# Kernel tuning notes

Measured on AMD Instinct MI355X. Metric: run time of the kernel, lower is better.

The kernel has to match this reference:

```python
import jax, jax.numpy as jnp
import numpy as np

OUT_SIZE = 7
SPATIAL_SCALE = 0.0625
SAMPLE_NUM = 2


def setup_inputs() -> dict:
    key = jax.random.key(0)
    k1, k2, k3, k4, k5, k6 = jax.random.split(key, 6)
    N, C, H, W = 4, 256, 96, 96
    K = 1024
    features = jax.random.normal(k1, (N, C, H, W), dtype=jnp.float32)
    img_h, img_w = H / SPATIAL_SCALE, W / SPATIAL_SCALE
    batch_idx = jax.random.randint(k2, (K,), 0, N).astype(jnp.float32)
    x1 = jax.random.uniform(k3, (K,)) * (img_w - 320.0)
    y1 = jax.random.uniform(k4, (K,)) * (img_h - 320.0)
    x2 = x1 + 16.0 + jax.random.uniform(k5, (K,)) * 300.0
    y2 = y1 + 16.0 + jax.random.uniform(k6, (K,)) * 300.0
    rois = jnp.stack([batch_idx, x1, y1, x2, y2], axis=1).astype(jnp.float32)
    return {"features": features, "rois": rois}


def _sample_coords(start, bin_size):
    # start, bin_size: [K]; returns [K, OUT_SIZE*SAMPLE_NUM] sample-point coords
    g = jnp.arange(OUT_SIZE * SAMPLE_NUM, dtype=jnp.float32)
    bin_idx = jnp.floor(g / SAMPLE_NUM)
    sub = g - bin_idx * SAMPLE_NUM
    offs = bin_idx + (sub + 0.5) / SAMPLE_NUM
    return start[:, None] + bin_size[:, None] * offs[None, :]


def _interp_1d(coord, size):
    # coord: [K, G] sample coords along one axis of a map of length `size`.
    valid = (coord >= -1.0) & (coord <= jnp.float32(size))
    c = jnp.clip(coord, 0.0, jnp.float32(size - 1))
    lo = jnp.floor(c)
    hi = jnp.minimum(lo + 1.0, jnp.float32(size - 1))
    frac = c - lo  # weight of hi; (1-frac) weight of lo
    return lo.astype(jnp.int32), hi.astype(jnp.int32), frac, valid


def roi_align(features, rois):
    N, C, H, W = features.shape
    b = rois[:, 0].astype(jnp.int32)
    x1, y1, x2, y2 = (rois[:, i] * SPATIAL_SCALE for i in (1, 2, 3, 4))
    roi_w = jnp.maximum(x2 - x1, 1.0)
    roi_h = jnp.maximum(y2 - y1, 1.0)
    bin_w = roi_w / OUT_SIZE
    bin_h = roi_h / OUT_SIZE

    ys = _sample_coords(y1, bin_h)  # [K, G]
    xs = _sample_coords(x1, bin_w)  # [K, G]
    ylo, yhi, fy, vy = _interp_1d(ys, H)
    xlo, xhi, fx, vx = _interp_1d(xs, W)

    bb = b[:, None, None]

    def gather(yi, xi):
        # -> [K, G, G, C]
        return features[bb, :, yi[:, :, None], xi[:, None, :]]

    wy_lo, wy_hi = (1.0 - fy), fy
    wx_lo, wx_hi = (1.0 - fx), fx

    def w2(wy, wx):
        return (wy[:, :, None] * wx[:, None, :])[..., None]

    val = (gather(ylo, xlo) * w2(wy_lo, wx_lo)
           + gather(ylo, xhi) * w2(wy_lo, wx_hi)
           + gather(yhi, xlo) * w2(wy_hi, wx_lo)
           + gather(yhi, xhi) * w2(wy_hi, wx_hi))
    mask = (vy[:, :, None] & vx[:, None, :])[..., None]
    val = jnp.where(mask, val, 0.0)

    K = rois.shape[0]
    G = OUT_SIZE * SAMPLE_NUM
    val = val.reshape(K, OUT_SIZE, SAMPLE_NUM, OUT_SIZE, SAMPLE_NUM, C)
    out = val.mean(axis=(2, 4))          # average the sample points per bin
    return jnp.transpose(out, (0, 3, 1, 2))  # [K, C, out, out]


def reference(features, rois):
    return roi_align(features, rois)
```

## Files before the change

kernel.cpp:

```cpp
#include <hip/hip_runtime.h>

#define CCH   256
#define FH    96
#define FW    96
#define HW    (FH*FW)
#define SCALE 0.0625f

#define HROWS 21
#define PSTR  28
#define PLANE (HROWS*PSTR)
#define WCH   32

__global__ __launch_bounds__(256, 8)
void roialign_kernel(const float* __restrict__ feat,
                     const float* __restrict__ rois,
                     float* __restrict__ out)
{
    __shared__ __align__(16) float win[4 * PLANE];
    __shared__ int   s_lo[2][14];
    __shared__ float s_wl[2][14], s_wh[2][14];

    const int k    = blockIdx.x >> 1;
    const int half = blockIdx.x & 1;
    const int tid  = threadIdx.x;
    const int w    = tid >> 6;
    const int ll   = tid & 63;

    const float x1 = rois[k*5+1] * SCALE;
    const float y1 = rois[k*5+2] * SCALE;
    const float x2 = rois[k*5+3] * SCALE;
    const float y2 = rois[k*5+4] * SCALE;
    const int   b  = (int)rois[k*5+0];
    const float binw = fmaxf(x2 - x1, 1.0f) * (1.0f/7.0f);
    const float binh = fmaxf(y2 - y1, 1.0f) * (1.0f/7.0f);

    if (tid < 28) {
        const int   axis  = (tid >= 14) ? 1 : 0;
        const int   g     = axis ? tid - 14 : tid;
        const float start = axis ? x1 : y1;
        const float bsz   = axis ? binw : binh;
        const float offs  = (float)(g >> 1) + 0.25f + 0.5f*(float)(g & 1);
        const float coord = start + bsz * offs;
        const bool  valid = (coord >= -1.0f) && (coord <= 96.0f);
        const float cc    = fminf(fmaxf(coord, 0.0f), 95.0f);
        const float lof   = floorf(cc);
        const float frac  = cc - lof;
        const float v     = valid ? 1.0f : 0.0f;
        s_lo[axis][g] = (int)lof;
        s_wl[axis][g] = (1.0f - frac) * v;
        s_wh[axis][g] = frac * v;
    }
    __syncthreads();

    const int row0 = s_lo[0][0];
    const int col0 = min(s_lo[1][0] & ~3, FW - 24);
    int hw_        = min(s_lo[0][13] + 1, FH-1) - row0 + 1;
    const int hwin = min(hw_, HROWS);
    const int nslot = hwin * 6;

    float* const wp = &win[w * PLANE];

    {
        const float4 z = make_float4(0.f, 0.f, 0.f, 0.f);
        #pragma unroll
        for (int j = 0; j < 3; ++j) {
            const int q = ll + 64*j;
            if (q < PLANE/4) *(float4*)&wp[q*4] = z;
        }
    }

    const bool active = ll < 49;
    const int  p  = active ? ll : 0;
    const int  oy = p / 7;
    const int  ox = p - oy*7;

    int   aL[4], aH[4];
    float w00[4], w01[4], w10[4], w11[4];
    #pragma unroll
    for (int sy = 0; sy < 2; ++sy) {
        const int   gy  = 2*oy + sy;
        const int   rlo = min(s_lo[0][gy] - row0,                 HROWS-1);
        const int   rhi = min(min(s_lo[0][gy]+1, FH-1) - row0,    HROWS-1);
        const float wyl = s_wl[0][gy], wyh = s_wh[0][gy];
        #pragma unroll
        for (int sx = 0; sx < 2; ++sx) {
            const int   gx  = 2*ox + sx;
            const int   clo = min(s_lo[1][gx] - col0, PSTR-2);
            const float wxl = s_wl[1][gx], wxh = s_wh[1][gx];
            const int   s   = sy*2 + sx;
            aL[s] = rlo*PSTR + clo;
            aH[s] = rhi*PSTR + clo;
            w00[s] = wyl*wxl*0.25f;  w01[s] = wyl*wxh*0.25f;
            w10[s] = wyh*wxl*0.25f;  w11[s] = wyh*wxh*0.25f;
        }
    }

    const int  sl1 = ll + 64;
    const int  r0  = ll  / 6, q0 = ll  - r0*6;
    const int  r1  = sl1 / 6, q1 = sl1 - r1*6;
    const bool L0  = ll  < nslot;
    const bool L1  = sl1 < nslot;
    const int  goff0 = min(row0 + r0, FH-1)*FW + col0 + q0*4;
    const int  goff1 = min(row0 + r1, FH-1)*FW + col0 + q1*4;
    const int  ld0   = min(r0, HROWS-1)*PSTR + q0*4;
    const int  ld1   = min(r1, HROWS-1)*PSTR + q1*4;

    const int    cb   = half*128 + w*WCH;
    const float* gch  = feat + (size_t)(b*CCH + cb) * HW;
    float*       outp = out  + ((size_t)k*CCH + cb)*49 + p;

    float4 st0, st1;
    if (L0) st0 = *(const float4*)(gch + goff0);
    if (L1) st1 = *(const float4*)(gch + goff1);

    for (int c = 0; c < WCH; ++c) {
        if (L0) *(float4*)&wp[ld0] = st0;
        if (L1) *(float4*)&wp[ld1] = st1;

        if (c + 1 < WCH) {
            const float* gn = gch + (size_t)(c+1)*HW;
            if (L0) st0 = *(const float4*)(gn + goff0);
            if (L1) st1 = *(const float4*)(gn + goff1);
        }

        if (active) {
            float acc = 0.0f;
            #pragma unroll
            for (int s = 0; s < 4; ++s) {
                acc += w00[s]*wp[aL[s]]   + w01[s]*wp[aL[s]+1]
                     + w10[s]*wp[aH[s]]   + w11[s]*wp[aH[s]+1];
            }
            outp[0] = acc;
        }
        outp += 49;
    }
}

extern "C" void kernel_launch(void* const* d_in, const int* in_sizes, int n_in,
                              void* d_out, int out_size, void* d_ws, size_t ws_size,
                              hipStream_t stream) {
    const float* feat = (const float*)d_in[0];
    const float* rois = (const float*)d_in[1];
    float*       outp = (float*)d_out;
    const int K = in_sizes[1] / 5;
    roialign_kernel<<<K*2, 256, 0, stream>>>(feat, rois, outp);
}
```

Baseline: 134.9 us.

## Prefetch four channels ahead, remap workgroups across XCDs, relax launch bounds

Each wave now keeps four channel windows in flight in registers instead of one, so global loads for later channels overlap the shared-memory store and bilinear compute of the current one. The per-channel sum is split into four independent partial sums to shorten the dependency chain. Workgroup IDs are remapped so that consecutive IDs, which round-robin across XCDs, are assigned to ROI/half pairs grouped per XCD. Launch bounds drop from 8 to 6 waves to leave room for the extra registers. The remap formula hardcodes K=1024, and the register pressure may lower occupancy.

```diff
diff --git a/kernel.cpp b/kernel.cpp
--- a/kernel.cpp
+++ b/kernel.cpp
@@ -11,7 +11,7 @@
 #define PLANE (HROWS*PSTR)
 #define WCH   32
 
-__global__ __launch_bounds__(256, 8)
+__global__ __launch_bounds__(256, 6)
 void roialign_kernel(const float* __restrict__ feat,
                      const float* __restrict__ rois,
                      float* __restrict__ out)
@@ -20,8 +20,10 @@
     __shared__ int   s_lo[2][14];
     __shared__ float s_wl[2][14], s_wh[2][14];
 
-    const int k    = blockIdx.x >> 1;
-    const int half = blockIdx.x & 1;
+    const int wgid = blockIdx.x;
+    const int k    = (wgid & 7) * 128 + (wgid >> 4);
+    const int half = (wgid >> 3) & 1;
+
     const int tid  = threadIdx.x;
     const int w    = tid >> 6;
     const int ll   = tid & 63;
@@ -109,30 +111,49 @@
     const float* gch  = feat + (size_t)(b*CCH + cb) * HW;
     float*       outp = out  + ((size_t)k*CCH + cb)*49 + p;
 
-    float4 st0, st1;
-    if (L0) st0 = *(const float4*)(gch + goff0);
-    if (L1) st1 = *(const float4*)(gch + goff1);
+    float4 pA0, pA1, pB0, pB1, pC0, pC1, pD0, pD1;
+    {
+        const float* g0 = gch;
+        if (L0) pA0 = *(const float4*)(g0 + goff0);
+        if (L1) pA1 = *(const float4*)(g0 + goff1);
+        const float* g1 = gch + HW;
+        if (L0) pB0 = *(const float4*)(g1 + goff0);
+        if (L1) pB1 = *(const float4*)(g1 + goff1);
+        const float* g2 = gch + 2*HW;
+        if (L0) pC0 = *(const float4*)(g2 + goff0);
+        if (L1) pC1 = *(const float4*)(g2 + goff1);
+        const float* g3 = gch + 3*HW;
+        if (L0) pD0 = *(const float4*)(g3 + goff0);
+        if (L1) pD1 = *(const float4*)(g3 + goff1);
+    }
 
-    for (int c = 0; c < WCH; ++c) {
-        if (L0) *(float4*)&wp[ld0] = st0;
-        if (L1) *(float4*)&wp[ld1] = st1;
-
-        if (c + 1 < WCH) {
-            const float* gn = gch + (size_t)(c+1)*HW;
-            if (L0) st0 = *(const float4*)(gn + goff0);
-            if (L1) st1 = *(const float4*)(gn + goff1);
+    auto chan = [&](float4 &s0, float4 &s1, int cnext) {
+        if (L0) *(float4*)&wp[ld0] = s0;
+        if (L1) *(float4*)&wp[ld1] = s1;
+        if (cnext < WCH) {
+            const float* gn = gch + (size_t)cnext * HW;
+            if (L0) s0 = *(const float4*)(gn + goff0);
+            if (L1) s1 = *(const float4*)(gn + goff1);
         }
-
         if (active) {
-            float acc = 0.0f;
-            #pragma unroll
-            for (int s = 0; s < 4; ++s) {
-                acc += w00[s]*wp[aL[s]]   + w01[s]*wp[aL[s]+1]
-                     + w10[s]*wp[aH[s]]   + w11[s]*wp[aH[s]+1];
-            }
-            outp[0] = acc;
+            float t0 = w00[0]*wp[aL[0]] + w01[0]*wp[aL[0]+1]
+                     + w10[0]*wp[aH[0]] + w11[0]*wp[aH[0]+1];
+            float t1 = w00[1]*wp[aL[1]] + w01[1]*wp[aL[1]+1]
+                     + w10[1]*wp[aH[1]] + w11[1]*wp[aH[1]+1];
+            float t2 = w00[2]*wp[aL[2]] + w01[2]*wp[aL[2]+1]
+                     + w10[2]*wp[aH[2]] + w11[2]*wp[aH[2]+1];
+            float t3 = w00[3]*wp[aL[3]] + w01[3]*wp[aL[3]+1]
+                     + w10[3]*wp[aH[3]] + w11[3]*wp[aH[3]+1];
+            outp[0] = (t0 + t1) + (t2 + t3);
         }
         outp += 49;
+    };
+
+    for (int c = 0; c < WCH; c += 4) {
+        chan(pA0, pA1, c + 4);
+        chan(pB0, pB1, c + 5);
+        chan(pC0, pC1, c + 6);
+        chan(pD0, pD1, c + 7);
     }
 }
 
```

Result: slower. 152.2 us (+12.8%).

## Separate bilinear pooling: reduce rows in registers before LDS, columns from LDS

Applied to the files above, without the earlier changes.

Each lane now fetches the four feature rows its output row needs and collapses the vertical interpolation and sample averaging in registers. It writes only a 7-row partial plane to shared memory, and the horizontal pass reads four values per output instead of sixteen. Two channels of loads are kept in flight, and the occupancy hint drops from 8 to 6 waves per SIMD to leave room for the extra registers. The aim is less LDS traffic and fewer FMAs per output. The cost is more, partly duplicated, global loads when sample rows overlap, plus higher register pressure.

```diff
diff --git a/kernel.cpp b/kernel.cpp
--- a/kernel.cpp
+++ b/kernel.cpp
@@ -6,12 +6,11 @@
 #define HW    (FH*FW)
 #define SCALE 0.0625f
 
-#define HROWS 21
-#define PSTR  28
-#define PLANE (HROWS*PSTR)
+#define RSTR  28
+#define PLANE (7*RSTR)
 #define WCH   32
 
-__global__ __launch_bounds__(256, 8)
+__global__ __launch_bounds__(256, 6)
 void roialign_kernel(const float* __restrict__ feat,
                      const float* __restrict__ rois,
                      float* __restrict__ out)
@@ -45,94 +44,93 @@
         const float cc    = fminf(fmaxf(coord, 0.0f), 95.0f);
         const float lof   = floorf(cc);
         const float frac  = cc - lof;
-        const float v     = valid ? 1.0f : 0.0f;
+        const float v     = valid ? (axis ? 1.0f : 0.25f) : 0.0f;
         s_lo[axis][g] = (int)lof;
         s_wl[axis][g] = (1.0f - frac) * v;
         s_wh[axis][g] = frac * v;
     }
     __syncthreads();
 
-    const int row0 = s_lo[0][0];
     const int col0 = min(s_lo[1][0] & ~3, FW - 24);
-    int hw_        = min(s_lo[0][13] + 1, FH-1) - row0 + 1;
-    const int hwin = min(hw_, HROWS);
-    const int nslot = hwin * 6;
 
     float* const wp = &win[w * PLANE];
 
-    {
-        const float4 z = make_float4(0.f, 0.f, 0.f, 0.f);
-        #pragma unroll
-        for (int j = 0; j < 3; ++j) {
-            const int q = ll + 64*j;
-            if (q < PLANE/4) *(float4*)&wp[q*4] = z;
-        }
+    if (ll < PLANE/4) {
+        *(float4*)&wp[ll*4] = make_float4(0.f, 0.f, 0.f, 0.f);
     }
 
     const bool active = ll < 49;
     const int  p  = active ? ll : 0;
     const int  oy = p / 7;
     const int  ox = p - oy*7;
-
-    int   aL[4], aH[4];
-    float w00[4], w01[4], w10[4], w11[4];
-    #pragma unroll
-    for (int sy = 0; sy < 2; ++sy) {
-        const int   gy  = 2*oy + sy;
-        const int   rlo = min(s_lo[0][gy] - row0,                 HROWS-1);
-        const int   rhi = min(min(s_lo[0][gy]+1, FH-1) - row0,    HROWS-1);
-        const float wyl = s_wl[0][gy], wyh = s_wh[0][gy];
-        #pragma unroll
-        for (int sx = 0; sx < 2; ++sx) {
-            const int   gx  = 2*ox + sx;
-            const int   clo = min(s_lo[1][gx] - col0, PSTR-2);
-            const float wxl = s_wl[1][gx], wxh = s_wh[1][gx];
-            const int   s   = sy*2 + sx;
-            aL[s] = rlo*PSTR + clo;
-            aH[s] = rhi*PSTR + clo;
-            w00[s] = wyl*wxl*0.25f;  w01[s] = wyl*wxh*0.25f;
-            w10[s] = wyh*wxl*0.25f;  w11[s] = wyh*wxh*0.25f;
-        }
+    float cw0, cw1, cw2, cw3;
+    int   ca0, ca1;
+    {
+        const int gx0 = 2*ox, gx1 = 2*ox + 1;
+        const int c0  = min(s_lo[1][gx0] - col0, 24);
+        const int c1  = min(s_lo[1][gx1] - col0, 24);
+        cw0 = s_wl[1][gx0];  cw1 = s_wh[1][gx0];
+        cw2 = s_wl[1][gx1];  cw3 = s_wh[1][gx1];
+        ca0 = oy*RSTR + c0;
+        ca1 = oy*RSTR + c1;
     }
 
-    const int  sl1 = ll + 64;
-    const int  r0  = ll  / 6, q0 = ll  - r0*6;
-    const int  r1  = sl1 / 6, q1 = sl1 - r1*6;
-    const bool L0  = ll  < nslot;
-    const bool L1  = sl1 < nslot;
-    const int  goff0 = min(row0 + r0, FH-1)*FW + col0 + q0*4;
-    const int  goff1 = min(row0 + r1, FH-1)*FW + col0 + q1*4;
-    const int  ld0   = min(r0, HROWS-1)*PSTR + q0*4;
-    const int  ld1   = min(r1, HROWS-1)*PSTR + q1*4;
+    const int  s   = min(ll, 41);
+    const int  soy = s / 6;
+    const int  sq  = s - soy*6;
+    const bool st  = ll < 42;
+    float sw0, sw1, sw2, sw3;
+    int   g0, g1, g2, g3;
+    {
+        const int gy0 = 2*soy, gy1 = 2*soy + 1;
+        const int rl0 = s_lo[0][gy0], rh0 = min(rl0 + 1, FH-1);
+        const int rl1 = s_lo[0][gy1], rh1 = min(rl1 + 1, FH-1);
+        sw0 = s_wl[0][gy0];  sw1 = s_wh[0][gy0];
+        sw2 = s_wl[0][gy1];  sw3 = s_wh[0][gy1];
+        const int cq = col0 + 4*sq;
+        g0 = rl0*FW + cq;  g1 = rh0*FW + cq;
+        g2 = rl1*FW + cq;  g3 = rh1*FW + cq;
+    }
+    const int ld = soy*RSTR + 4*sq;
 
     const int    cb   = half*128 + w*WCH;
     const float* gch  = feat + (size_t)(b*CCH + cb) * HW;
     float*       outp = out  + ((size_t)k*CCH + cb)*49 + p;
 
-    float4 st0, st1;
-    if (L0) st0 = *(const float4*)(gch + goff0);
-    if (L1) st1 = *(const float4*)(gch + goff1);
+    float4 A0, A1, A2, A3, B0, B1, B2, B3;
+    {
+        const float* ga = gch;
+        A0 = *(const float4*)(ga + g0);  A1 = *(const float4*)(ga + g1);
+        A2 = *(const float4*)(ga + g2);  A3 = *(const float4*)(ga + g3);
+        const float* gb = gch + HW;
+        B0 = *(const float4*)(gb + g0);  B1 = *(const float4*)(gb + g1);
+        B2 = *(const float4*)(gb + g2);  B3 = *(const float4*)(gb + g3);
+    }
 
-    for (int c = 0; c < WCH; ++c) {
-        if (L0) *(float4*)&wp[ld0] = st0;
-        if (L1) *(float4*)&wp[ld1] = st1;
+    auto chan = [&](float4& R0, float4& R1, float4& R2, float4& R3, int cnext) {
+        float4 v;
+        v.x = sw0*R0.x + sw1*R1.x + sw2*R2.x + sw3*R3.x;
+        v.y = sw0*R0.y + sw1*R1.y + sw2*R2.y + sw3*R3.y;
+        v.z = sw0*R0.z + sw1*R1.z + sw2*R2.z + sw3*R3.z;
+        v.w = sw0*R0.w + sw1*R1.w + sw2*R2.w + sw3*R3.w;
+        if (st) *(float4*)&wp[ld] = v;
 
-        if (c + 1 < WCH) {
-            const float* gn = gch + (size_t)(c+1)*HW;
-            if (L0) st0 = *(const float4*)(gn + goff0);
-            if (L1) st1 = *(const float4*)(gn + goff1);
+        if (cnext < WCH) {
+            const float* gn = gch + (size_t)cnext * HW;
+            R0 = *(const float4*)(gn + g0);  R1 = *(const float4*)(gn + g1);
+            R2 = *(const float4*)(gn + g2);  R3 = *(const float4*)(gn + g3);
         }
 
         if (active) {
-            float acc = 0.0f;
-            #pragma unroll
-            for (int s = 0; s < 4; ++s) {
-                acc += w00[s]*wp[aL[s]]   + w01[s]*wp[aL[s]+1]
-                     + w10[s]*wp[aH[s]]   + w11[s]*wp[aH[s]+1];
-            }
-            outp[0] = acc;
+            outp[0] = cw0*wp[ca0] + cw1*wp[ca0+1]
+                    + cw2*wp[ca1] + cw3*wp[ca1+1];
         }
         outp += 49;
+    };
+
+    for (int c = 0; c < WCH; c += 2) {
+        chan(A0, A1, A2, A3, c + 2);
+        chan(B0, B1, B2, B3, c + 3);
     }
 }
 
```

Measured after the change: 149.3 us. +10.7%, slower.
